# Kernel tuning notes

Measured on AMD Instinct MI355X. Metric: run time of the kernel, lower is better.

## Reference

```python
import jax, jax.numpy as jnp
import numpy as np

KEY_SIZE = 256
EPS = 1e-8  # torch F.cosine_similarity default eps


def setup_inputs() -> dict:
    key = jax.random.key(0)
    k1, k2 = jax.random.split(key)
    B, M, K, V = 2048, 100000, KEY_SIZE, 256
    query = jax.random.normal(k1, (B, K), dtype=jnp.float32)
    memory = jax.random.normal(k2, (M, K + V), dtype=jnp.float32)
    return {"query": query, "memory": memory}


def reference(query, memory):
    # memory: [M, K+V] -> keys [M, K], values [M, V]
    keys = memory[:, :KEY_SIZE]
    values = memory[:, KEY_SIZE:]
    # cosine similarity: (q . k) / max(|q|*|k|, eps)  -> [B, M]
    dots = jnp.einsum('bk,mk->bm', query, keys)
    qn = jnp.linalg.norm(query, axis=1)  # [B]
    kn = jnp.linalg.norm(keys, axis=1)   # [M]
    sims = dots / jnp.maximum(qn[:, None] * kn[None, :], EPS)
    # top-1 over memory dim, then gather values -> [B, V]
    idx = jnp.argmax(sims, axis=1)
    return values[idx]
```

## Files before the change

kernel.cpp:

```cpp
#include <hip/hip_runtime.h>
#include <hip/hip_fp16.h>
#include <float.h>

#define MKEY 256
#define NMEM 100000
#define NPAD 100096
#define NQ   2048
#define BM 128
#define BN 128
#define NTILES 782
#define BLKPAD 800
#define MTILES 16
#define GRID (128 * 98)
#define KEYBLOCKS (NPAD / 4)
#define QS (127.0f / 6.0f)
#define SS2 ((6.0f / 127.0f) * (6.0f / 127.0f))

typedef int i32x4 __attribute__((ext_vector_type(4)));

__device__ inline void gll16(const void* g, void* l) {
  __builtin_amdgcn_global_load_lds(
      (const __attribute__((address_space(1))) unsigned*)g,
      (__attribute__((address_space(3))) unsigned*)l, 16, 0, 0);
}

__device__ inline int pack_i8x4(float4 v) {
  int c0 = max(-127, min(127, __float2int_rn(v.x * QS)));
  int c1 = max(-127, min(127, __float2int_rn(v.y * QS)));
  int c2 = max(-127, min(127, __float2int_rn(v.z * QS)));
  int c3 = max(-127, min(127, __float2int_rn(v.w * QS)));
  return (c0 & 255) | ((c1 & 255) << 8) | ((c2 & 255) << 16) | ((c3 & 255) << 24);
}

__device__ inline int dot4i8(int a, int b, int s) {
#if __has_builtin(__builtin_amdgcn_sdot4)
  return __builtin_amdgcn_sdot4(a, b, s, false);
#else
#pragma unroll
  for (int k = 0; k < 4; ++k) {
    const int av = (a << (24 - 8 * k)) >> 24;
    const int bv = (b << (24 - 8 * k)) >> 24;
    s += av * bv;
  }
  return s;
#endif
}

__global__ void convert(const float* __restrict__ q, const float* __restrict__ mem,
                        int* __restrict__ qi, int* __restrict__ ki,
                        float* __restrict__ rkn) {
  const int b = blockIdx.x;
  if (b >= KEYBLOCKS) {
    const int i = (b - KEYBLOCKS) * 256 + threadIdx.x;
    const float4 v = *(const float4*)&q[(size_t)i * 4];
    qi[i] = pack_i8x4(v);
    return;
  }
  const int t = threadIdx.x, lane = t & 63, w = t >> 6;
  const int row = b * 4 + w;
  if (row < NMEM) {
    const float4 v = *(const float4*)&mem[(long)row * 512 + lane * 4];
    const float ss0 = v.x * v.x + v.y * v.y + v.z * v.z + v.w * v.w;
    ki[(size_t)row * 64 + lane] = pack_i8x4(v);
    float ss = ss0;
#pragma unroll
    for (int off = 32; off >= 1; off >>= 1) ss += __shfl_xor(ss, off, 64);
    if (lane == 0) rkn[row] = 1.0f / sqrtf(fmaxf(ss, 1e-30f));
  } else {
    ki[(size_t)row * 64 + lane] = 0;
    if (lane == 0) rkn[row] = 0.f;
  }
}

__global__ __launch_bounds__(256, 4) void gemm_screen(
    const int* __restrict__ qi, const int* __restrict__ ki,
    const float* __restrict__ rkn,
    float* __restrict__ bmax16B, float* __restrict__ bmaxB) {
  __shared__ __align__(128) char smem[33792];
  char* const Ab = smem;
  char* const Bb = smem + 16384;

  const int id = blockIdx.x;
  const int mtile = (id >> 3) & 15;
  const int ntile = (id & 7) + 8 * (id >> 7);
  if (ntile >= NTILES) return;

  const int t = threadIdx.x;
  const int w = t >> 6;
  const int lane = t & 63;
  const int wr = w >> 1, wc = w & 1;
  const int q16 = lane >> 4, l16 = lane & 15;
  const int l8 = lane >> 3, c8 = lane & 7;

  const int swz = (c8 ^ l8) * 16;
  int soff[8];
#pragma unroll
  for (int c = 0; c < 8; ++c)
    soff[c] = ((w & 1) * 64 + c * 8 + l8) * 256 + swz;
  const char* asrc = (const char*)((w < 2) ? qi : ki) +
                     (size_t)(((w < 2) ? mtile : ntile) * 128) * 256;
  char* adst = ((w < 2) ? Ab : Bb) + (w & 1) * 8192;

  i32x4 acc[4][4];
#pragma unroll
  for (int i = 0; i < 4; i++)
#pragma unroll
    for (int j = 0; j < 4; j++) acc[i][j] = (i32x4){0, 0, 0, 0};

  int pc[2];
#pragma unroll
  for (int ks = 0; ks < 2; ++ks) pc[ks] = (((ks * 4 + q16) ^ (l16 & 7))) * 16;

#pragma unroll
  for (int s = 0; s < 2; ++s) {
    __syncthreads();
#pragma unroll
    for (int c = 0; c < 8; ++c)
      gll16(asrc + s * 128 + soff[c], adst + c * 1024);
    __syncthreads();
#pragma unroll
    for (int ks = 0; ks < 2; ++ks) {
      i32x4 av[4], bv[4];
#pragma unroll
      for (int i = 0; i < 4; i++)
        av[i] = *(const i32x4*)&Ab[(64 * wr + 16 * i + l16) * 128 + pc[ks]];
#pragma unroll
      for (int j = 0; j < 4; j++)
        bv[j] = *(const i32x4*)&Bb[(64 * wc + 16 * j + l16) * 128 + pc[ks]];
#pragma unroll
      for (int i = 0; i < 4; i++)
#pragma unroll
        for (int j = 0; j < 4; j++)
          acc[i][j] = __builtin_amdgcn_mfma_i32_16x16x64_i8(av[i], bv[j], acc[i][j], 0, 0, 0);
    }
  }

  float rk[4];
#pragma unroll
  for (int j = 0; j < 4; j++) {
    const int ncol = ntile * BN + 64 * wc + 16 * j + l16;
    rk[j] = (ncol < NMEM) ? rkn[ncol] * SS2 : 0.f;
  }
  float (*L)[20] = (float(*)[20])smem;
  float* bhalf = (float*)(smem + 32768);
  const int wr_ = t >> 7, gg = (t >> 4) & 7, qrow = t & 15;
  float outv[4];
  __syncthreads();
#pragma unroll
  for (int i = 0; i < 4; ++i) {
#pragma unroll
    for (int j = 0; j < 4; ++j)
#pragma unroll
      for (int r = 0; r < 4; ++r)
        L[(wr * 8 + wc * 4 + j) * 16 + q16 * 4 + r][l16] = (float)acc[i][j][r] * rk[j];
    __syncthreads();
    const float* Lr = L[(wr_ * 8 + gg) * 16 + qrow];
    const float4 a = *(const float4*)&Lr[0], b4 = *(const float4*)&Lr[4];
    const float4 cc = *(const float4*)&Lr[8], dd = *(const float4*)&Lr[12];
    float m = fmaxf(fmaxf(fmaxf(a.x, a.y), fmaxf(a.z, a.w)),
                    fmaxf(fmaxf(b4.x, b4.y), fmaxf(b4.z, b4.w)));
    m = fmaxf(m, fmaxf(fmaxf(cc.x, cc.y), fmaxf(cc.z, cc.w)));
    m = fmaxf(m, fmaxf(fmaxf(dd.x, dd.y), fmaxf(dd.z, dd.w)));
    outv[i] = m;
    float bm = fmaxf(m, __shfl_xor(m, 16, 64));
    bm = fmaxf(bm, __shfl_xor(bm, 32, 64));
    if (lane < 16) bhalf[(w * 16 + lane) * 4 + i] = bm;
    __syncthreads();
  }
#pragma unroll
  for (int i = 0; i < 4; ++i)
    bmax16B[((size_t)ntile * NQ + mtile * 128 + wr_ * 64 + i * 16 + qrow) * 8 + gg] =
        outv[i];
  if (t < 128) {
    const int wrb = t >> 6, ib = (t >> 4) & 3, qr = t & 15;
    const float v = fmaxf(bhalf[((2 * wrb) * 16 + qr) * 4 + ib],
                          bhalf[((2 * wrb + 1) * 16 + qr) * 4 + ib]);
    bmaxB[(size_t)ntile * NQ + mtile * 128 + t] = v;
  }
}

__global__ __launch_bounds__(256) void transpose_blk(const float* __restrict__ in,
                                                     float* __restrict__ outp) {
  __shared__ float tl[32][33];
  const int bid = blockIdx.x;
  const int ntt = bid % 25, qt = bid / 25;
  const int r0 = ntt * 32, c0 = qt * 32;
  const int tx = threadIdx.x & 31, ty = threadIdx.x >> 5;
#pragma unroll
  for (int k = 0; k < 4; ++k) {
    const int r = r0 + ty + 8 * k;
    tl[ty + 8 * k][tx] = (r < NTILES) ? in[(size_t)r * NQ + c0 + tx] : -FLT_MAX;
  }
  __syncthreads();
#pragma unroll
  for (int k = 0; k < 4; ++k) {
    const int qq = c0 + ty + 8 * k;
    const int nt = r0 + tx;
    if (nt < NTILES) outp[(size_t)qq * BLKPAD + nt] = tl[tx][ty + 8 * k];
  }
}

__global__ __launch_bounds__(256) void rescore_gather(
    const float* __restrict__ q, const float* __restrict__ mem,
    const int* __restrict__ qi8, const int* __restrict__ ki8,
    const float* __restrict__ rkn, const float* __restrict__ bmaxQ,
    const float* __restrict__ bmax16B, float* __restrict__ out) {
  __shared__ float red2[4];
  __shared__ int blist[64];
  __shared__ int nblk;
  __shared__ int glist[128];
  __shared__ int ng;
  __shared__ int rlist[256];
  __shared__ int nrow;
  __shared__ double wb[4];
  __shared__ int wbi[4];
  __shared__ int widx;

  const int qid = blockIdx.x;
  const int t = threadIdx.x, w = t >> 6, lane = t & 63;

  const float4 qv = *(const float4*)&q[(size_t)qid * 256 + lane * 4];
  float ss = qv.x * qv.x + qv.y * qv.y + qv.z * qv.z + qv.w * qv.w;
#pragma unroll
  for (int off = 32; off >= 1; off >>= 1) ss += __shfl_xor(ss, off, 64);
  const float qn = sqrtf(ss);
  const float margin = 1.8e-2f * qn;

  int4 qreg[4];
#pragma unroll
  for (int k = 0; k < 4; ++k)
    qreg[k] = *(const int4*)&qi8[(size_t)qid * 64 + (lane & 3) * 16 + k * 4];

  if (t == 0) { nblk = 0; ng = 0; nrow = 0; }
  const float* bq = &bmaxQ[(size_t)qid * BLKPAD];

  float gm = -FLT_MAX;
  for (int i = t; i < NTILES; i += 256) gm = fmaxf(gm, bq[i]);
#pragma unroll
  for (int off = 32; off >= 1; off >>= 1) gm = fmaxf(gm, __shfl_xor(gm, off, 64));
  if (lane == 0) red2[w] = gm;
  __syncthreads();
  gm = fmaxf(fmaxf(red2[0], red2[1]), fmaxf(red2[2], red2[3]));
  const float thresh = gm - margin;

  for (int i = t; i < NTILES; i += 256)
    if (bq[i] >= thresh) {
      int p = atomicAdd(&nblk, 1);
      if (p < 64) blist[p] = i;
    }
  __syncthreads();
  const int nb_ = min(nblk, 64);

  for (int idx = t; idx < nb_ * 8; idx += 256) {
    const int nt = blist[idx >> 3], gl = idx & 7;
    if (bmax16B[((size_t)nt * NQ + qid) * 8 + gl] >= thresh) {
      int p = atomicAdd(&ng, 1);
      if (p < 128) glist[p] = nt * 8 + gl;
    }
  }
  __syncthreads();
  const int ng_ = min(ng, 128);

  for (int c = w; c < ng_; c += 4) {
    const int row = glist[c] * 16 + (lane >> 2);
    int idot = 0;
#pragma unroll
    for (int k = 0; k < 4; ++k) {
      const int4 kv = *(const int4*)&ki8[(size_t)row * 64 + (lane & 3) * 16 + k * 4];
      idot = dot4i8(kv.x, qreg[k].x, idot);
      idot = dot4i8(kv.y, qreg[k].y, idot);
      idot = dot4i8(kv.z, qreg[k].z, idot);
      idot = dot4i8(kv.w, qreg[k].w, idot);
    }
    idot += __shfl_xor(idot, 1, 64);
    idot += __shfl_xor(idot, 2, 64);
    if ((lane & 3) == 0 && row < NMEM) {
      const float sh = (float)idot * (rkn[row] * SS2);
      if (sh >= thresh) {
        int p = atomicAdd(&nrow, 1);
        if (p < 256) rlist[p] = row;
      }
    }
  }
  __syncthreads();
  const int nr = min(nrow, 256);

  double bestv = -1e300;
  int bestidx = 0x7fffffff;
  for (int c = w; c < nr; c += 4) {
    const int row = rlist[c];
    const float4 kv = *(const float4*)&mem[(size_t)row * 512 + lane * 4];
    double d = (double)kv.x * qv.x + (double)kv.y * qv.y +
               (double)kv.z * qv.z + (double)kv.w * qv.w;
    double s2 = (double)kv.x * kv.x + (double)kv.y * kv.y +
                (double)kv.z * kv.z + (double)kv.w * kv.w;
#pragma unroll
    for (int off = 32; off >= 1; off >>= 1) {
      d += __shfl_xor(d, off, 64);
      s2 += __shfl_xor(s2, off, 64);
    }
    if (lane == 0) {
      const double score = d / sqrt(s2 > 1e-300 ? s2 : 1e-300);
      if (score > bestv || (score == bestv && row < bestidx)) {
        bestv = score;
        bestidx = row;
      }
    }
  }
  if (lane == 0) { wb[w] = bestv; wbi[w] = bestidx; }
  __syncthreads();
  if (t == 0) {
    double bv = wb[0];
    int bi = wbi[0];
#pragma unroll
    for (int w2 = 1; w2 < 4; ++w2)
      if (wb[w2] > bv || (wb[w2] == bv && wbi[w2] < bi)) {
        bv = wb[w2];
        bi = wbi[w2];
      }
    widx = bi;
  }
  __syncthreads();
  out[(size_t)qid * 256 + t] = mem[(size_t)widx * 512 + 256 + t];
}

extern "C" void kernel_launch(void* const* d_in, const int* in_sizes, int n_in,
                              void* d_out, int out_size, void* d_ws, size_t ws_size,
                              hipStream_t stream) {
  const float* query = (const float*)d_in[0];
  const float* memory = (const float*)d_in[1];
  float* out = (float*)d_out;

  char* p = (char*)d_ws;
  int* qi = (int*)p; p += (size_t)NQ * 64 * 4;
  int* ki = (int*)p; p += (size_t)NPAD * 64 * 4;
  float* rkn = (float*)p; p += (size_t)NPAD * 4;
  float* bmaxB = (float*)p; p += (size_t)NTILES * NQ * 4;
  float* bmaxQ = (float*)p; p += (size_t)NQ * BLKPAD * 4;
  float* bmax16B = (float*)p; p += (size_t)NTILES * NQ * 32;

  hipLaunchKernelGGL(convert, dim3(KEYBLOCKS + NQ * MKEY / 1024), dim3(256), 0, stream,
                     query, memory, qi, ki, rkn);
  hipLaunchKernelGGL(gemm_screen, dim3(GRID), dim3(256), 0, stream,
                     qi, ki, rkn, bmax16B, bmaxB);
  hipLaunchKernelGGL(transpose_blk, dim3(25 * 64), dim3(256), 0, stream, bmaxB, bmaxQ);
  hipLaunchKernelGGL(rescore_gather, dim3(NQ), dim3(256), 0, stream,
                     query, memory, qi, ki, rkn, bmaxQ, bmax16B, out);
}
```

Baseline: 369.0 us.

## Compress per-group maxima to 8-bit codes and double-buffer GEMM K-staging

The screening GEMM now stores per-16-column group maxima as 8-bit quantized gaps below the 128-column block maximum, packed into one 64-bit word per query and tile. This replaces the 32-byte float record and cuts global write and read traffic between the GEMM and the rescore kernel. The K loop is also split into four 64-byte stages with double-buffered LDS staging, so the next stage's loads overlap the current MFMAs. The quantized codes round the gap down, and a small epsilon in the threshold test keeps selection conservative, which may let a few extra groups through for rescoring.

```diff
diff --git a/kernel.cpp b/kernel.cpp
--- a/kernel.cpp
+++ b/kernel.cpp
@@ -10,11 +10,12 @@
 #define BN 128
 #define NTILES 782
 #define BLKPAD 800
-#define MTILES 16
 #define GRID (128 * 98)
 #define KEYBLOCKS (NPAD / 4)
 #define QS (127.0f / 6.0f)
 #define SS2 ((6.0f / 127.0f) * (6.0f / 127.0f))
+#define GDELTA 0.04f
+#define GINVD  25.0f
 
 typedef int i32x4 __attribute__((ext_vector_type(4)));
 
@@ -75,10 +76,8 @@
 __global__ __launch_bounds__(256, 4) void gemm_screen(
     const int* __restrict__ qi, const int* __restrict__ ki,
     const float* __restrict__ rkn,
-    float* __restrict__ bmax16B, float* __restrict__ bmaxB) {
+    unsigned long long* __restrict__ bcode8, float* __restrict__ bmaxB) {
   __shared__ __align__(128) char smem[33792];
-  char* const Ab = smem;
-  char* const Bb = smem + 16384;
 
   const int id = blockIdx.x;
   const int mtile = (id >> 3) & 15;
@@ -90,16 +89,24 @@
   const int lane = t & 63;
   const int wr = w >> 1, wc = w & 1;
   const int q16 = lane >> 4, l16 = lane & 15;
-  const int l8 = lane >> 3, c8 = lane & 7;
-
-  const int swz = (c8 ^ l8) * 16;
-  int soff[8];
-#pragma unroll
-  for (int c = 0; c < 8; ++c)
-    soff[c] = ((w & 1) * 64 + c * 8 + l8) * 256 + swz;
-  const char* asrc = (const char*)((w < 2) ? qi : ki) +
-                     (size_t)(((w < 2) ? mtile : ntile) * 128) * 256;
-  char* adst = ((w < 2) ? Ab : Bb) + (w & 1) * 8192;
+
+  const int swz64 = ((lane & 3) ^ ((lane >> 2) & 3)) * 16;
+  int soff4[4];
+#pragma unroll
+  for (int c = 0; c < 4; ++c)
+    soff4[c] = ((w & 1) * 64 + c * 16 + (lane >> 2)) * 256 + swz64;
+  const char* const asrc = (const char*)((w < 2) ? qi : ki) +
+                           (size_t)(((w < 2) ? mtile : ntile) * 128) * 256;
+  char* const dbase = smem + ((w < 2) ? 0 : 16384) + (w & 1) * 4096;
+
+#define STG(p, s)                                         \
+  do {                                                    \
+    const char* _s = asrc + (s) * 64;                     \
+    char* _d = dbase + (p) * 8192;                        \
+    _Pragma("unroll")                                     \
+    for (int c = 0; c < 4; ++c)                           \
+      gll16(_s + soff4[c], _d + c * 1024);                \
+  } while (0)
 
   i32x4 acc[4][4];
 #pragma unroll
@@ -107,33 +114,29 @@
 #pragma unroll
     for (int j = 0; j < 4; j++) acc[i][j] = (i32x4){0, 0, 0, 0};
 
-  int pc[2];
-#pragma unroll
-  for (int ks = 0; ks < 2; ++ks) pc[ks] = (((ks * 4 + q16) ^ (l16 & 7))) * 16;
-
-#pragma unroll
-  for (int s = 0; s < 2; ++s) {
+  const int pc4 = (q16 ^ (l16 & 3)) * 16;
+
+  STG(0, 0);
+  __syncthreads();
+#pragma unroll
+  for (int s = 0; s < 4; ++s) {
+    if (s < 3) STG((s + 1) & 1, s + 1);
+    const int p = (s & 1) * 8192;
+    i32x4 av[4], bv[4];
+#pragma unroll
+    for (int i = 0; i < 4; i++)
+      av[i] = *(const i32x4*)&smem[p + (64 * wr + 16 * i + l16) * 64 + pc4];
+#pragma unroll
+    for (int j = 0; j < 4; j++)
+      bv[j] = *(const i32x4*)&smem[16384 + p + (64 * wc + 16 * j + l16) * 64 + pc4];
+#pragma unroll
+    for (int i = 0; i < 4; i++)
+#pragma unroll
+      for (int j = 0; j < 4; j++)
+        acc[i][j] = __builtin_amdgcn_mfma_i32_16x16x64_i8(av[i], bv[j], acc[i][j], 0, 0, 0);
     __syncthreads();
-#pragma unroll
-    for (int c = 0; c < 8; ++c)
-      gll16(asrc + s * 128 + soff[c], adst + c * 1024);
-    __syncthreads();
-#pragma unroll
-    for (int ks = 0; ks < 2; ++ks) {
-      i32x4 av[4], bv[4];
-#pragma unroll
-      for (int i = 0; i < 4; i++)
-        av[i] = *(const i32x4*)&Ab[(64 * wr + 16 * i + l16) * 128 + pc[ks]];
-#pragma unroll
-      for (int j = 0; j < 4; j++)
-        bv[j] = *(const i32x4*)&Bb[(64 * wc + 16 * j + l16) * 128 + pc[ks]];
-#pragma unroll
-      for (int i = 0; i < 4; i++)
-#pragma unroll
-        for (int j = 0; j < 4; j++)
-          acc[i][j] = __builtin_amdgcn_mfma_i32_16x16x64_i8(av[i], bv[j], acc[i][j], 0, 0, 0);
-    }
-  }
+  }
+#undef STG
 
   float rk[4];
 #pragma unroll
@@ -145,7 +148,6 @@
   float* bhalf = (float*)(smem + 32768);
   const int wr_ = t >> 7, gg = (t >> 4) & 7, qrow = t & 15;
   float outv[4];
-  __syncthreads();
 #pragma unroll
   for (int i = 0; i < 4; ++i) {
 #pragma unroll
@@ -167,16 +169,27 @@
     if (lane < 16) bhalf[(w * 16 + lane) * 4 + i] = bm;
     __syncthreads();
   }
-#pragma unroll
-  for (int i = 0; i < 4; ++i)
-    bmax16B[((size_t)ntile * NQ + mtile * 128 + wr_ * 64 + i * 16 + qrow) * 8 + gg] =
-        outv[i];
+  float* brow = (float*)smem;
+  unsigned char* cb = (unsigned char*)(smem + 512);
   if (t < 128) {
     const int wrb = t >> 6, ib = (t >> 4) & 3, qr = t & 15;
     const float v = fmaxf(bhalf[((2 * wrb) * 16 + qr) * 4 + ib],
                           bhalf[((2 * wrb + 1) * 16 + qr) * 4 + ib]);
+    brow[t] = v;
     bmaxB[(size_t)ntile * NQ + mtile * 128 + t] = v;
   }
+  __syncthreads();
+#pragma unroll
+  for (int i = 0; i < 4; ++i) {
+    const int row = wr_ * 64 + i * 16 + qrow;
+    int code = (int)((brow[row] - outv[i]) * GINVD);
+    code = min(255, max(0, code));
+    cb[row * 8 + gg] = (unsigned char)code;
+  }
+  __syncthreads();
+  if (t < 128)
+    bcode8[(size_t)ntile * NQ + mtile * 128 + t] =
+        *(const unsigned long long*)&cb[t * 8];
 }
 
 __global__ __launch_bounds__(256) void transpose_blk(const float* __restrict__ in,
@@ -204,7 +217,7 @@
     const float* __restrict__ q, const float* __restrict__ mem,
     const int* __restrict__ qi8, const int* __restrict__ ki8,
     const float* __restrict__ rkn, const float* __restrict__ bmaxQ,
-    const float* __restrict__ bmax16B, float* __restrict__ out) {
+    const unsigned long long* __restrict__ bcode8, float* __restrict__ out) {
   __shared__ float red2[4];
   __shared__ int blist[64];
   __shared__ int nblk;
@@ -253,7 +266,9 @@
 
   for (int idx = t; idx < nb_ * 8; idx += 256) {
     const int nt = blist[idx >> 3], gl = idx & 7;
-    if (bmax16B[((size_t)nt * NQ + qid) * 8 + gl] >= thresh) {
+    const unsigned long long cw = bcode8[(size_t)nt * NQ + qid];
+    const int code = (int)((cw >> (8 * gl)) & 255);
+    if ((float)code * GDELTA <= bq[nt] - thresh + 1e-6f) {
       int p = atomicAdd(&ng, 1);
       if (p < 128) glist[p] = nt * 8 + gl;
     }
@@ -337,13 +352,14 @@
   float* rkn = (float*)p; p += (size_t)NPAD * 4;
   float* bmaxB = (float*)p; p += (size_t)NTILES * NQ * 4;
   float* bmaxQ = (float*)p; p += (size_t)NQ * BLKPAD * 4;
-  float* bmax16B = (float*)p; p += (size_t)NTILES * NQ * 32;
+  unsigned long long* bcode8 = (unsigned long long*)p;
+  p += (size_t)NTILES * NQ * 8;
 
   hipLaunchKernelGGL(convert, dim3(KEYBLOCKS + NQ * MKEY / 1024), dim3(256), 0, stream,
                      query, memory, qi, ki, rkn);
   hipLaunchKernelGGL(gemm_screen, dim3(GRID), dim3(256), 0, stream,
-                     qi, ki, rkn, bmax16B, bmaxB);
+                     qi, ki, rkn, bcode8, bmaxB);
   hipLaunchKernelGGL(transpose_blk, dim3(25 * 64), dim3(256), 0, stream, bmaxB, bmaxQ);
   hipLaunchKernelGGL(rescore_gather, dim3(NQ), dim3(256), 0, stream,
-                     query, memory, qi, ki, rkn, bmaxQ, bmax16B, out);
-}
+                     query, memory, qi, ki, rkn, bmaxQ, bcode8, out);
+}
```

Result: no change. 362.8 us (-1.7%).
